# Kernel tuning notes

Measured on AMD Instinct MI355X. Metric: run time of the kernel, lower is better.

Reference implementation:

```python
import jax, jax.numpy as jnp
import numpy as np

B, T, C, H = 2, 2048, 1024, 16
HD = C // H          # head_dim = 64
HALF = HD // 2       # rope half dim = 32
ROPE_BASE = 10000.0


def _build_sin_cos(seq_len, half_dim, base=ROPE_BASE):
    # mirrors build_sin_cos: angles[t, i] = t * base^(-2i / (2*half_dim))
    pos = jnp.arange(seq_len, dtype=jnp.float32)[:, None]                     # [T,1]
    inv_freq = 1.0 / (base ** (jnp.arange(0, half_dim * 2, 2, dtype=jnp.float32) / (half_dim * 2)))
    angles = pos * inv_freq                                                   # [T, half]
    return jnp.sin(angles), jnp.cos(angles)


def setup_inputs() -> dict:
    key = jax.random.key(0)
    k1, k2, k3 = jax.random.split(key, 3)
    x = jax.random.normal(k1, (B, T, C), dtype=jnp.float32)
    # nn.Linear weights (stored as [out,in] in torch; we keep [in,out] for x @ W)
    Wqkv = jax.random.normal(k2, (C, 3 * C), dtype=jnp.float32) * (C ** -0.5)
    Wproj = jax.random.normal(k3, (C, C), dtype=jnp.float32) * (C ** -0.5)
    rope_sin, rope_cos = _build_sin_cos(T, HALF)
    return {"x": x, "Wqkv": Wqkv, "Wproj": Wproj, "rope_sin": rope_sin, "rope_cos": rope_cos}


def reference(x, Wqkv, Wproj, rope_sin, rope_cos):
    Bb, Tt, Cc = x.shape
    Hh = H
    hd = Cc // Hh
    # fused QKV projection, then per-head split (matches view(B,T,H,3*hd).split)
    qkv = (x @ Wqkv).reshape(Bb, Tt, Hh, 3 * hd)
    q, k, v = jnp.split(qkv, 3, axis=-1)                                      # each [B,T,H,hd]
    # RoPE (single device path: local slice == full range)
    s = rope_sin[:Tt][None, :, None, :].astype(x.dtype)                       # [1,T,1,half]
    c = rope_cos[:Tt][None, :, None, :].astype(x.dtype)

    def rot(t):
        t1, t2 = jnp.split(t, 2, axis=-1)
        return jnp.concatenate([t1 * c - t2 * s, t1 * s + t2 * c], axis=-1)

    q = rot(q)
    k = rot(k)
    # causal scaled dot-product attention (flash_attn default scale = hd^-0.5)
    scale = jnp.asarray(hd, x.dtype) ** -0.5
    scores = jnp.einsum('bqhd,bkhd->bhqk', q, k) * scale                      # [B,H,T,T]
    causal = jnp.tril(jnp.ones((Tt, Tt), dtype=bool))
    scores = jnp.where(causal, scores, jnp.finfo(x.dtype).min)
    probs = jax.nn.softmax(scores, axis=-1)
    attn = jnp.einsum('bhqk,bkhd->bqhd', probs, v).reshape(Bb, Tt, Cc)
    return attn @ Wproj
```

## Files before the change

### kernel.cpp

```cpp
#include <hip/hip_runtime.h>

#define Bb 2
#define Tt 2048
#define Cc_ 1024
#define Hh 16
#define HDd 64

typedef __attribute__((ext_vector_type(8))) short bf16x8;
typedef __attribute__((ext_vector_type(4))) float f32x4;
typedef __attribute__((ext_vector_type(4))) unsigned short u16x4;
typedef __attribute__((ext_vector_type(2))) unsigned int u32x2;

__device__ __forceinline__ unsigned short f2bf(float f) {
  union { float f; unsigned int u; } v; v.f = f;
  unsigned int r = v.u + 0x7FFFu + ((v.u >> 16) & 1u);
  return (unsigned short)(r >> 16);
}
__device__ __forceinline__ float bf2f(unsigned short u) {
  union { unsigned int u; float f; } v; v.u = ((unsigned int)u) << 16;
  return v.f;
}
__device__ __forceinline__ unsigned int cvtpk(float lo, float hi) {
  unsigned int r;
  asm("v_cvt_pk_bf16_f32 %0, %1, %2" : "=v"(r) : "v"(lo), "v"(hi));
  return r;
}
__device__ __forceinline__ f32x4 mfma16(bf16x8 a, bf16x8 b, f32x4 c) {
  return __builtin_amdgcn_mfma_f32_16x16x32_bf16(a, b, c, 0, 0, 0);
}
__device__ __forceinline__ void gl_lds16(const void* g, void* l) {
  auto* gp = reinterpret_cast<const __attribute__((address_space(1))) unsigned int*>(
      reinterpret_cast<unsigned long long>(g));
  auto* lp = reinterpret_cast<__attribute__((address_space(3))) unsigned int*>(
      reinterpret_cast<unsigned long long>(l));
  __builtin_amdgcn_global_load_lds(gp, lp, 16, 0, 0);
}

__global__ __launch_bounds__(256) void k_prep(const float* __restrict__ x,
                                              const float* __restrict__ Wqkv,
                                              const float* __restrict__ Wproj,
                                              unsigned short* __restrict__ xb,
                                              unsigned short* __restrict__ wqkvt,
                                              unsigned short* __restrict__ wprot) {
  const int bid = blockIdx.x;
  const int tid = threadIdx.x;
  if (bid < 4096) {
    const int i = bid * 256 + tid;
    f32x4 v = ((const f32x4*)x)[i];
    u16x4 o;
    o[0] = f2bf(v[0]); o[1] = f2bf(v[1]); o[2] = f2bf(v[2]); o[3] = f2bf(v[3]);
    ((u16x4*)xb)[i] = o;
    return;
  }
  __shared__ float tile[32][33];
  const int tx = tid & 31, ty = tid >> 5;
  if (bid < 4096 + 3072) {
    const int tt = bid - 4096;
    const int n0 = (tt % 96) * 32, k0 = (tt / 96) * 32;
    const int region = n0 >> 10, nl = n0 & 1023;
    const int ob = (nl >> 6) * 192 + region * 64 + (nl & 63);
#pragma unroll
    for (int i = 0; i < 4; ++i)
      tile[ty + i * 8][tx] = Wqkv[(size_t)(k0 + ty + i * 8) * 3072 + ob + tx];
    __syncthreads();
#pragma unroll
    for (int i = 0; i < 4; ++i)
      wqkvt[(size_t)(n0 + ty + i * 8) * 1024 + k0 + tx] = f2bf(tile[tx][ty + i * 8]);
    return;
  }
  const int tt = bid - 7168;
  const int c0 = (tt & 31) * 32, r0 = (tt >> 5) * 32;
#pragma unroll
  for (int i = 0; i < 4; ++i)
    tile[ty + i * 8][tx] = Wproj[(size_t)(r0 + ty + i * 8) * 1024 + c0 + tx];
  __syncthreads();
#pragma unroll
  for (int i = 0; i < 4; ++i)
    wprot[(size_t)(c0 + ty + i * 8) * 1024 + r0 + tx] = f2bf(tile[tx][ty + i * 8]);
}

__global__ __launch_bounds__(256) void k_gemm_qkv(const unsigned short* __restrict__ A,
                                                  const unsigned short* __restrict__ Bt,
                                                  const float* __restrict__ rsin,
                                                  const float* __restrict__ rcos,
                                                  unsigned short* __restrict__ Qo,
                                                  unsigned short* __restrict__ Ko,
                                                  unsigned short* __restrict__ Vt) {
  __shared__ unsigned short lA[2][128 * 64];
  __shared__ unsigned short lB[2][128 * 64];
  const int K = 1024;
  const int tid = threadIdx.x;
  const int lane = tid & 63, wid = tid >> 6;
  const int wr = wid >> 1, wc = wid & 1;
  const int bm = blockIdx.y * 128, bn = blockIdx.x * 128;
  const int l15 = lane & 15, l4 = lane >> 4;
  f32x4 acc[4][4];
#pragma unroll
  for (int i = 0; i < 4; ++i)
#pragma unroll
    for (int j = 0; j < 4; ++j) acc[i][j] = f32x4{0.f, 0.f, 0.f, 0.f};

#define STG(BUF, TT)                                                        \
  {                                                                         \
    const int k0 = (TT) << 6;                                               \
    _Pragma("unroll") for (int i = 0; i < 4; ++i) {                         \
      const int slot = i * 256 + tid;                                       \
      const int row = slot >> 3, g = slot & 7;                              \
      const int gs = (g ^ (row & 7)) * 8;                                   \
      gl_lds16(A + (size_t)(bm + row) * K + k0 + gs, &lA[BUF][slot * 8]);   \
      gl_lds16(Bt + (size_t)(bn + row) * K + k0 + gs, &lB[BUF][slot * 8]);  \
    }                                                                       \
  }

  STG(0, 0);
  asm volatile("s_waitcnt vmcnt(0)" ::: "memory");
  __builtin_amdgcn_s_barrier();
  for (int t = 0; t < 16; ++t) {
    const int cur = t & 1;
    if (t + 1 < 16) STG(cur ^ 1, t + 1);
    __builtin_amdgcn_s_setprio(1);
#pragma unroll
    for (int ks = 0; ks < 2; ++ks) {
      bf16x8 af[4], bfr[4];
#pragma unroll
      for (int mf = 0; mf < 4; ++mf) {
        const int row = wr * 64 + mf * 16 + l15;
        const int g = ks * 4 + l4;
        af[mf] = *(const bf16x8*)&lA[cur][row * 64 + ((g ^ (row & 7)) * 8)];
      }
#pragma unroll
      for (int nf = 0; nf < 4; ++nf) {
        const int row = wc * 64 + nf * 16 + l15;
        const int g = ks * 4 + l4;
        bfr[nf] = *(const bf16x8*)&lB[cur][row * 64 + ((g ^ (row & 7)) * 8)];
      }
#pragma unroll
      for (int mf = 0; mf < 4; ++mf)
#pragma unroll
        for (int nf = 0; nf < 4; ++nf)
          acc[mf][nf] = mfma16(af[mf], bfr[nf], acc[mf][nf]);
    }
    __builtin_amdgcn_s_setprio(0);
    if (t + 1 < 16) asm volatile("s_waitcnt vmcnt(0)" ::: "memory");
    __builtin_amdgcn_s_barrier();
  }
#undef STG

  const int rb = bm + wr * 64 + l4 * 4;
  const int region = blockIdx.x >> 3;
  if (region < 2) {
    const int h = (blockIdx.x & 7) * 2 + wc;
    unsigned short* dst = (region == 0) ? Qo : Ko;
    const float qs = (region == 0) ? (0.125f * 1.44269504088896f) : 1.0f;
#pragma unroll
    for (int mf = 0; mf < 4; ++mf)
#pragma unroll
      for (int j = 0; j < 4; ++j) {
        const int trow = rb + mf * 16 + j;
        const int bi = trow >> 11, t = trow & 2047;
        const size_t rowb = ((size_t)(bi * Hh + h) * Tt + t) * 64;
#pragma unroll
        for (int nf = 0; nf < 2; ++nf) {
          const int d = nf * 16 + l15;
          const float sn = rsin[t * 32 + d], cs = rcos[t * 32 + d];
          const float a1 = acc[mf][nf][j], a2 = acc[mf][nf + 2][j];
          dst[rowb + d] = f2bf((a1 * cs - a2 * sn) * qs);
          dst[rowb + d + 32] = f2bf((a1 * sn + a2 * cs) * qs);
        }
      }
  } else {
    unsigned short* tp = &lA[0][0];
    const int h0 = (blockIdx.x & 7) * 2;
    const int bi = bm >> 11, tbase = bm & 2047;
    const int dd = tid >> 2, t0c = (tid & 3) * 32;
#pragma unroll
    for (int ph = 0; ph < 2; ++ph) {
      if (wc == ph) {
#pragma unroll
        for (int mf = 0; mf < 4; ++mf)
#pragma unroll
          for (int nf = 0; nf < 4; ++nf)
#pragma unroll
            for (int j = 0; j < 4; ++j) {
              const int tl = wr * 64 + mf * 16 + l4 * 4 + j;
              const int dl = nf * 16 + l15;
              tp[tl * 65 + dl] = f2bf(acc[mf][nf][j]);
            }
      }
      __syncthreads();
      const size_t ob = ((size_t)(bi * Hh + h0 + ph) * 64 + dd) * (size_t)Tt + tbase + t0c;
#pragma unroll
      for (int c = 0; c < 8; ++c) {
        u16x4 v4;
#pragma unroll
        for (int e = 0; e < 4; ++e) v4[e] = tp[(t0c + c * 4 + e) * 65 + dd];
        *(u16x4*)&Vt[ob + c * 4] = v4;
      }
      __syncthreads();
    }
  }
}

__global__ __launch_bounds__(256, 4) void k_attn(const unsigned short* __restrict__ Q,
                                                 const unsigned short* __restrict__ Kt,
                                                 const unsigned short* __restrict__ Vt,
                                                 unsigned short* __restrict__ Aout) {
  __shared__ unsigned short lK[2 * 64 * 64];
  __shared__ unsigned short lV[2 * 64 * 64];
  __shared__ unsigned short lP[4 * 16 * 64];
  const int bid = blockIdx.x;
  const int xcd = bid & 7, ss = bid >> 3;
  const int cc = ss & 31, kk = ss >> 5;
  const int bh = xcd * 4 + kk;
  const int c2 = (cc + ((kk & 2) ? 16 : 0)) & 31;
  const int qt = (kk & 1) ? (31 - c2) : c2;
  const int b = bh >> 4, h = bh & 15;
  const int tid = threadIdx.x, lane = tid & 63, w = tid >> 6;
  const int l15 = lane & 15, l4 = lane >> 4;
  const int qb = qt * 64;
  const unsigned short* Kbh = Kt + (size_t)bh * Tt * 64;
  const unsigned short* Vbh = Vt + (size_t)bh * 64 * Tt;

  int fo[4][2];
#pragma unroll
  for (int a = 0; a < 4; ++a)
#pragma unroll
    for (int bb = 0; bb < 2; ++bb)
      fo[a][bb] = ((a * 16 + l15) * 64 + (((bb * 4 + l4) ^ (l15 & 7)) * 8)) * 2;
  int pwo[4];
#pragma unroll
  for (int nf = 0; nf < 4; ++nf)
    pwo[nf] = (l15 * 64 + (((nf * 2 + (l4 >> 1)) ^ (l15 & 7)) * 8) + (l4 & 1) * 4) * 2;
  char* const pB = (char*)lP + w * 2048;
  char* const kB0 = (char*)lK;
  char* const vB0 = (char*)lV;
  const int rA = tid >> 3;
  const int gsA = ((tid & 7) ^ (rA & 7)) * 8;
  const int kgA = rA * 64 + gsA;
  const int vgA = rA * 2048 + gsA;
  char* const ldKA = (char*)lK + tid * 16;
  char* const ldVA = (char*)lV + tid * 16;

#define STAGE(BUF, TT)                                                   \
  {                                                                      \
    const int kv_ = (TT) * 64;                                           \
    gl_lds16(Kbh + kv_ * 64 + kgA, ldKA + (BUF) * 8192);                 \
    gl_lds16(Kbh + kv_ * 64 + kgA + 32 * 64, ldKA + (BUF) * 8192 + 4096);\
    gl_lds16(Vbh + kv_ + vgA, ldVA + (BUF) * 8192);                      \
    gl_lds16(Vbh + kv_ + vgA + 32 * 2048, ldVA + (BUF) * 8192 + 4096);   \
  }

  const size_t qoff = ((size_t)bh * Tt + qb + w * 16 + l15) * 64 + l4 * 8;
  const bf16x8 qf0 = *(const bf16x8*)&Q[qoff];
  const bf16x8 qf1 = *(const bf16x8*)&Q[qoff + 32];
  f32x4 o[4];
#pragma unroll
  for (int i = 0; i < 4; ++i) o[i] = f32x4{0.f, 0.f, 0.f, 0.f};
  float mrun = -1e30f, lrun = 0.f;
  const int nt = qt + 1;

#define BODY(CUR, T, LASTT)                                                       \
  {                                                                               \
    if ((T) + 1 < nt) STAGE(CUR ^ 1, (T) + 1);                                    \
    f32x4 sv[4];                                                                  \
    _Pragma("unroll") for (int i = 0; i < 4; ++i) sv[i] = f32x4{0.f, 0.f, 0.f, 0.f}; \
    __builtin_amdgcn_s_setprio(1);                                                \
    _Pragma("unroll") for (int ks = 0; ks < 2; ++ks) {                            \
      const bf16x8 qa = ks ? qf1 : qf0;                                           \
      _Pragma("unroll") for (int nf = 0; nf < 4; ++nf) {                          \
        const bf16x8 kf = *(const bf16x8*)(kB0 + (CUR) * 8192 + fo[nf][ks]);      \
        sv[nf] = mfma16(kf, qa, sv[nf]);                                          \
      }                                                                           \
    }                                                                             \
    __builtin_amdgcn_s_setprio(0);                                                \
    if (LASTT) {                                                                  \
      _Pragma("unroll") for (int nf = 0; nf < 4; ++nf)                            \
        _Pragma("unroll") for (int j = 0; j < 4; ++j)                             \
          if (nf * 16 + l4 * 4 + j > w * 16 + l15) sv[nf][j] = -3e38f;            \
    }                                                                             \
    float mx = fmaxf(fmaxf(fmaxf(sv[0][0], sv[0][1]), fmaxf(sv[0][2], sv[0][3])), \
                     fmaxf(fmaxf(sv[1][0], sv[1][1]), fmaxf(sv[1][2], sv[1][3])));\
    mx = fmaxf(mx, fmaxf(fmaxf(fmaxf(sv[2][0], sv[2][1]), fmaxf(sv[2][2], sv[2][3])), \
                         fmaxf(fmaxf(sv[3][0], sv[3][1]), fmaxf(sv[3][2], sv[3][3])))); \
    if (!__all(mx - mrun <= 8.0f)) {                                              \
      mx = fmaxf(mx, __shfl_xor(mx, 16, 64));                                     \
      mx = fmaxf(mx, __shfl_xor(mx, 32, 64));                                     \
      const float mnew = fmaxf(mrun, mx);                                         \
      const float alpha = exp2f(mrun - mnew);                                     \
      lrun *= alpha;                                                              \
      float aj[4];                                                                \
      _Pragma("unroll") for (int j = 0; j < 4; ++j) aj[j] = __shfl(alpha, l4 * 4 + j, 64); \
      _Pragma("unroll") for (int df = 0; df < 4; ++df)                            \
        _Pragma("unroll") for (int j = 0; j < 4; ++j) o[df][j] *= aj[j];          \
      mrun = mnew;                                                                \
    }                                                                             \
    _Pragma("unroll") for (int nf = 0; nf < 4; ++nf) {                            \
      const float p0 = exp2f(sv[nf][0] - mrun), p1 = exp2f(sv[nf][1] - mrun);     \
      const float p2 = exp2f(sv[nf][2] - mrun), p3 = exp2f(sv[nf][3] - mrun);     \
      lrun += (p0 + p1) + (p2 + p3);                                              \
      u32x2 pk; pk[0] = cvtpk(p0, p1); pk[1] = cvtpk(p2, p3);                     \
      *(u32x2*)(pB + pwo[nf]) = pk;                                               \
    }                                                                             \
    __builtin_amdgcn_s_setprio(1);                                                \
    _Pragma("unroll") for (int kb = 0; kb < 2; ++kb) {                            \
      const bf16x8 pa = *(const bf16x8*)(pB + fo[0][kb]);                         \
      _Pragma("unroll") for (int df = 0; df < 4; ++df) {                          \
        const bf16x8 vb = *(const bf16x8*)(vB0 + (CUR) * 8192 + fo[df][kb]);      \
        o[df] = mfma16(pa, vb, o[df]);                                            \
      }                                                                           \
    }                                                                             \
    __builtin_amdgcn_s_setprio(0);                                                \
    if ((T) + 1 < nt) asm volatile("s_waitcnt vmcnt(0)" ::: "memory");            \
    __builtin_amdgcn_s_barrier();                                                 \
  }

  STAGE(0, 0);
  asm volatile("s_waitcnt vmcnt(0)" ::: "memory");
  __builtin_amdgcn_s_barrier();
  int t = 0;
  for (; t + 2 < nt; t += 2) {
    BODY(0, t, false);
    BODY(1, t + 1, false);
  }
  if (nt - t == 2) {
    BODY(0, t, false);
    BODY(1, t + 1, true);
  } else {
    BODY(0, t, true);
  }
#undef BODY
#undef STAGE

  lrun += __shfl_xor(lrun, 16, 64);
  lrun += __shfl_xor(lrun, 32, 64);
  const float rinv = 1.f / lrun;
  float lj[4];
#pragma unroll
  for (int j = 0; j < 4; ++j) lj[j] = __shfl(rinv, l4 * 4 + j, 64);
#pragma unroll
  for (int j = 0; j < 4; ++j) {
    const size_t rr = (size_t)(b * Tt + qb + w * 16 + l4 * 4 + j) * 1024 + h * 64 + l15;
#pragma unroll
    for (int df = 0; df < 4; ++df) Aout[rr + df * 16] = f2bf(o[df][j] * lj[j]);
  }
}

__global__ __launch_bounds__(256) void k_gemm2(const unsigned short* __restrict__ A,
                                               const unsigned short* __restrict__ Bt,
                                               float* __restrict__ Cout) {
  __shared__ unsigned short lA[2][128 * 64];
  __shared__ unsigned short lB[2][64 * 64];
  const int K = 1024, N = 1024;
  const int tid = threadIdx.x;
  const int lane = tid & 63, w = tid >> 6;
  const int bm = blockIdx.y * 128, bn = blockIdx.x * 64;
  const int l15 = lane & 15, l4 = lane >> 4;
  f32x4 acc[2][4];
#pragma unroll
  for (int i = 0; i < 2; ++i)
#pragma unroll
    for (int j = 0; j < 4; ++j) acc[i][j] = f32x4{0.f, 0.f, 0.f, 0.f};

#define STG(BUF, TT)                                                        \
  {                                                                         \
    const int k0 = (TT) << 6;                                               \
    _Pragma("unroll") for (int i = 0; i < 4; ++i) {                         \
      const int slot = i * 256 + tid;                                       \
      const int row = slot >> 3, g = slot & 7;                              \
      const int gs = (g ^ (row & 7)) * 8;                                   \
      gl_lds16(A + (size_t)(bm + row) * K + k0 + gs, &lA[BUF][slot * 8]);   \
    }                                                                       \
    _Pragma("unroll") for (int i = 0; i < 2; ++i) {                         \
      const int slot = i * 256 + tid;                                       \
      const int row = slot >> 3, g = slot & 7;                              \
      const int gs = (g ^ (row & 7)) * 8;                                   \
      gl_lds16(Bt + (size_t)(bn + row) * K + k0 + gs, &lB[BUF][slot * 8]);  \
    }                                                                       \
  }

  STG(0, 0);
  asm volatile("s_waitcnt vmcnt(0)" ::: "memory");
  __builtin_amdgcn_s_barrier();
  for (int t = 0; t < 16; ++t) {
    const int cur = t & 1;
    if (t + 1 < 16) STG(cur ^ 1, t + 1);
    __builtin_amdgcn_s_setprio(1);
#pragma unroll
    for (int ks = 0; ks < 2; ++ks) {
      bf16x8 af[2], bfr[4];
#pragma unroll
      for (int mf = 0; mf < 2; ++mf) {
        const int row = w * 32 + mf * 16 + l15;
        const int g = ks * 4 + l4;
        af[mf] = *(const bf16x8*)&lA[cur][row * 64 + ((g ^ (row & 7)) * 8)];
      }
#pragma unroll
      for (int nf = 0; nf < 4; ++nf) {
        const int row = nf * 16 + l15;
        const int g = ks * 4 + l4;
        bfr[nf] = *(const bf16x8*)&lB[cur][row * 64 + ((g ^ (row & 7)) * 8)];
      }
#pragma unroll
      for (int mf = 0; mf < 2; ++mf)
#pragma unroll
        for (int nf = 0; nf < 4; ++nf)
          acc[mf][nf] = mfma16(af[mf], bfr[nf], acc[mf][nf]);
    }
    __builtin_amdgcn_s_setprio(0);
    if (t + 1 < 16) asm volatile("s_waitcnt vmcnt(0)" ::: "memory");
    __builtin_amdgcn_s_barrier();
  }
#undef STG
  const int rb = bm + w * 32 + l4 * 4;
  const int cb = bn + l15;
#pragma unroll
  for (int mf = 0; mf < 2; ++mf)
#pragma unroll
    for (int nf = 0; nf < 4; ++nf)
#pragma unroll
      for (int j = 0; j < 4; ++j)
        Cout[(size_t)(rb + mf * 16 + j) * N + cb + nf * 16] = acc[mf][nf][j];
}

extern "C" void kernel_launch(void* const* d_in, const int* in_sizes, int n_in,
                              void* d_out, int out_size, void* d_ws, size_t ws_size,
                              hipStream_t stream) {
  const float* x = (const float*)d_in[0];
  const float* Wqkv = (const float*)d_in[1];
  const float* Wproj = (const float*)d_in[2];
  const float* rsin = (const float*)d_in[3];
  const float* rcos = (const float*)d_in[4];
  float* out = (float*)d_out;
  char* ws = (char*)d_ws;
  unsigned short* xb = (unsigned short*)(ws);
  unsigned short* wqkvt = (unsigned short*)(ws + (size_t)(8 << 20));
  unsigned short* wprot = (unsigned short*)(ws + (size_t)(14 << 20));
  unsigned short* Q = (unsigned short*)(ws + (size_t)(40 << 20));
  unsigned short* K = (unsigned short*)(ws + (size_t)(48 << 20));
  unsigned short* Vt = (unsigned short*)(ws + (size_t)(56 << 20));
  unsigned short* attn = (unsigned short*)(ws + (size_t)(64 << 20));

  k_prep<<<8192, 256, 0, stream>>>(x, Wqkv, Wproj, xb, wqkvt, wprot);
  k_gemm_qkv<<<dim3(24, 32), 256, 0, stream>>>(xb, wqkvt, rsin, rcos, Q, K, Vt);
  k_attn<<<1024, 256, 0, stream>>>(Q, K, Vt, attn);
  k_gemm2<<<dim3(16, 32), 256, 0, stream>>>(attn, wprot, out);
}
```

Measured before the change: 176.2 us.

## Rewrite attention kernel with 32x32 MFMA, two waves, register P exchange

Switches the attention kernel from 16x16x32 to 32x32x16 bf16 MFMA tiles, with each of two waves owning 32 query rows instead of four waves with 16 rows each. The P matrix is no longer staged through LDS; the probabilities are packed to bf16 and swapped between half-waves with a cross-lane shuffle to form the A operand for the PV product. Row statistics are broadcast through a small LDS array. The aim is to cut LDS traffic and raise MFMA efficiency. The cost is fewer waves per block, higher register pressure from the 16-wide accumulators, and less latency hiding.

Measured after the change: 192.7 us. 1.09x slower.

```diff
diff --git a/kernel.cpp b/kernel.cpp
--- a/kernel.cpp
+++ b/kernel.cpp
@@ -8,6 +8,7 @@
 
 typedef __attribute__((ext_vector_type(8))) short bf16x8;
 typedef __attribute__((ext_vector_type(4))) float f32x4;
+typedef __attribute__((ext_vector_type(16))) float f32x16;
 typedef __attribute__((ext_vector_type(4))) unsigned short u16x4;
 typedef __attribute__((ext_vector_type(2))) unsigned int u32x2;
 
@@ -27,6 +28,9 @@
 }
 __device__ __forceinline__ f32x4 mfma16(bf16x8 a, bf16x8 b, f32x4 c) {
   return __builtin_amdgcn_mfma_f32_16x16x32_bf16(a, b, c, 0, 0, 0);
+}
+__device__ __forceinline__ f32x16 mfma32(bf16x8 a, bf16x8 b, f32x16 c) {
+  return __builtin_amdgcn_mfma_f32_32x32x16_bf16(a, b, c, 0, 0, 0);
 }
 __device__ __forceinline__ void gl_lds16(const void* g, void* l) {
   auto* gp = reinterpret_cast<const __attribute__((address_space(1))) unsigned int*>(
@@ -201,13 +205,13 @@
   }
 }
 
-__global__ __launch_bounds__(256, 4) void k_attn(const unsigned short* __restrict__ Q,
+__global__ __launch_bounds__(128, 2) void k_attn(const unsigned short* __restrict__ Q,
                                                  const unsigned short* __restrict__ Kt,
                                                  const unsigned short* __restrict__ Vt,
                                                  unsigned short* __restrict__ Aout) {
   __shared__ unsigned short lK[2 * 64 * 64];
   __shared__ unsigned short lV[2 * 64 * 64];
-  __shared__ unsigned short lP[4 * 16 * 64];
+  __shared__ float sred[2][32];
   const int bid = blockIdx.x;
   const int xcd = bid & 7, ss = bid >> 3;
   const int cc = ss & 31, kk = ss >> 5;
@@ -216,102 +220,116 @@
   const int qt = (kk & 1) ? (31 - c2) : c2;
   const int b = bh >> 4, h = bh & 15;
   const int tid = threadIdx.x, lane = tid & 63, w = tid >> 6;
-  const int l15 = lane & 15, l4 = lane >> 4;
+  const int l31 = lane & 31, ht = lane >> 5, l7 = lane & 7;
   const int qb = qt * 64;
   const unsigned short* Kbh = Kt + (size_t)bh * Tt * 64;
   const unsigned short* Vbh = Vt + (size_t)bh * 64 * Tt;
 
-  int fo[4][2];
-#pragma unroll
-  for (int a = 0; a < 4; ++a)
-#pragma unroll
-    for (int bb = 0; bb < 2; ++bb)
-      fo[a][bb] = ((a * 16 + l15) * 64 + (((bb * 4 + l4) ^ (l15 & 7)) * 8)) * 2;
-  int pwo[4];
-#pragma unroll
-  for (int nf = 0; nf < 4; ++nf)
-    pwo[nf] = (l15 * 64 + (((nf * 2 + (l4 >> 1)) ^ (l15 & 7)) * 8) + (l4 & 1) * 4) * 2;
-  char* const pB = (char*)lP + w * 2048;
-  char* const kB0 = (char*)lK;
-  char* const vB0 = (char*)lV;
-  const int rA = tid >> 3;
-  const int gsA = ((tid & 7) ^ (rA & 7)) * 8;
-  const int kgA = rA * 64 + gsA;
-  const int vgA = rA * 2048 + gsA;
-  char* const ldKA = (char*)lK + tid * 16;
-  char* const ldVA = (char*)lV + tid * 16;
-
-#define STAGE(BUF, TT)                                                   \
-  {                                                                      \
-    const int kv_ = (TT) * 64;                                           \
-    gl_lds16(Kbh + kv_ * 64 + kgA, ldKA + (BUF) * 8192);                 \
-    gl_lds16(Kbh + kv_ * 64 + kgA + 32 * 64, ldKA + (BUF) * 8192 + 4096);\
-    gl_lds16(Vbh + kv_ + vgA, ldVA + (BUF) * 8192);                      \
-    gl_lds16(Vbh + kv_ + vgA + 32 * 2048, ldVA + (BUF) * 8192 + 4096);   \
-  }
-
-  const size_t qoff = ((size_t)bh * Tt + qb + w * 16 + l15) * 64 + l4 * 8;
-  const bf16x8 qf0 = *(const bf16x8*)&Q[qoff];
-  const bf16x8 qf1 = *(const bf16x8*)&Q[qoff + 32];
-  f32x4 o[4];
-#pragma unroll
-  for (int i = 0; i < 4; ++i) o[i] = f32x4{0.f, 0.f, 0.f, 0.f};
+  int off[2][4];
+#pragma unroll
+  for (int c = 0; c < 2; ++c)
+#pragma unroll
+    for (int g4 = 0; g4 < 4; ++g4)
+      off[c][g4] = (c * 32 + l31) * 64 + (((ht + g4 * 2) ^ l7) * 8);
+  const int rA = tid >> 3, gA = tid & 7;
+  const int sws = (gA ^ (rA & 7)) * 8;
+
+#define STAGE(BUF, TT)                                                              \
+  {                                                                                 \
+    const int kv_ = (TT) * 64;                                                      \
+    _Pragma("unroll") for (int i = 0; i < 4; ++i) {                                 \
+      const int row = rA + i * 16;                                                  \
+      gl_lds16(Kbh + (size_t)(kv_ + row) * 64 + sws, &lK[(BUF)*4096 + row * 64 + gA * 8]); \
+      gl_lds16(Vbh + (size_t)row * 2048 + kv_ + sws, &lV[(BUF)*4096 + row * 64 + gA * 8]); \
+    }                                                                               \
+  }
+
+  const size_t qrow_off = ((size_t)bh * Tt + qb + w * 32 + l31) * 64;
+  bf16x8 qf[4];
+#pragma unroll
+  for (int kd = 0; kd < 4; ++kd) qf[kd] = *(const bf16x8*)&Q[qrow_off + kd * 16 + ht * 8];
+
+  f32x16 o0, o1;
+#pragma unroll
+  for (int r = 0; r < 16; ++r) { o0[r] = 0.f; o1[r] = 0.f; }
   float mrun = -1e30f, lrun = 0.f;
   const int nt = qt + 1;
 
-#define BODY(CUR, T, LASTT)                                                       \
-  {                                                                               \
-    if ((T) + 1 < nt) STAGE(CUR ^ 1, (T) + 1);                                    \
-    f32x4 sv[4];                                                                  \
-    _Pragma("unroll") for (int i = 0; i < 4; ++i) sv[i] = f32x4{0.f, 0.f, 0.f, 0.f}; \
-    __builtin_amdgcn_s_setprio(1);                                                \
-    _Pragma("unroll") for (int ks = 0; ks < 2; ++ks) {                            \
-      const bf16x8 qa = ks ? qf1 : qf0;                                           \
-      _Pragma("unroll") for (int nf = 0; nf < 4; ++nf) {                          \
-        const bf16x8 kf = *(const bf16x8*)(kB0 + (CUR) * 8192 + fo[nf][ks]);      \
-        sv[nf] = mfma16(kf, qa, sv[nf]);                                          \
-      }                                                                           \
-    }                                                                             \
-    __builtin_amdgcn_s_setprio(0);                                                \
-    if (LASTT) {                                                                  \
-      _Pragma("unroll") for (int nf = 0; nf < 4; ++nf)                            \
-        _Pragma("unroll") for (int j = 0; j < 4; ++j)                             \
-          if (nf * 16 + l4 * 4 + j > w * 16 + l15) sv[nf][j] = -3e38f;            \
-    }                                                                             \
-    float mx = fmaxf(fmaxf(fmaxf(sv[0][0], sv[0][1]), fmaxf(sv[0][2], sv[0][3])), \
-                     fmaxf(fmaxf(sv[1][0], sv[1][1]), fmaxf(sv[1][2], sv[1][3])));\
-    mx = fmaxf(mx, fmaxf(fmaxf(fmaxf(sv[2][0], sv[2][1]), fmaxf(sv[2][2], sv[2][3])), \
-                         fmaxf(fmaxf(sv[3][0], sv[3][1]), fmaxf(sv[3][2], sv[3][3])))); \
-    if (!__all(mx - mrun <= 8.0f)) {                                              \
-      mx = fmaxf(mx, __shfl_xor(mx, 16, 64));                                     \
-      mx = fmaxf(mx, __shfl_xor(mx, 32, 64));                                     \
-      const float mnew = fmaxf(mrun, mx);                                         \
-      const float alpha = exp2f(mrun - mnew);                                     \
-      lrun *= alpha;                                                              \
-      float aj[4];                                                                \
-      _Pragma("unroll") for (int j = 0; j < 4; ++j) aj[j] = __shfl(alpha, l4 * 4 + j, 64); \
-      _Pragma("unroll") for (int df = 0; df < 4; ++df)                            \
-        _Pragma("unroll") for (int j = 0; j < 4; ++j) o[df][j] *= aj[j];          \
-      mrun = mnew;                                                                \
-    }                                                                             \
-    _Pragma("unroll") for (int nf = 0; nf < 4; ++nf) {                            \
-      const float p0 = exp2f(sv[nf][0] - mrun), p1 = exp2f(sv[nf][1] - mrun);     \
-      const float p2 = exp2f(sv[nf][2] - mrun), p3 = exp2f(sv[nf][3] - mrun);     \
-      lrun += (p0 + p1) + (p2 + p3);                                              \
-      u32x2 pk; pk[0] = cvtpk(p0, p1); pk[1] = cvtpk(p2, p3);                     \
-      *(u32x2*)(pB + pwo[nf]) = pk;                                               \
-    }                                                                             \
-    __builtin_amdgcn_s_setprio(1);                                                \
-    _Pragma("unroll") for (int kb = 0; kb < 2; ++kb) {                            \
-      const bf16x8 pa = *(const bf16x8*)(pB + fo[0][kb]);                         \
-      _Pragma("unroll") for (int df = 0; df < 4; ++df) {                          \
-        const bf16x8 vb = *(const bf16x8*)(vB0 + (CUR) * 8192 + fo[df][kb]);      \
-        o[df] = mfma16(pa, vb, o[df]);                                            \
-      }                                                                           \
-    }                                                                             \
-    __builtin_amdgcn_s_setprio(0);                                                \
-    if ((T) + 1 < nt) asm volatile("s_waitcnt vmcnt(0)" ::: "memory");            \
-    __builtin_amdgcn_s_barrier();                                                 \
+#define BODY(CUR, T, LASTT)                                                             \
+  {                                                                                     \
+    if ((T) + 1 < nt) STAGE(CUR ^ 1, (T) + 1);                                          \
+    f32x16 s0, s1;                                                                      \
+    _Pragma("unroll") for (int r = 0; r < 16; ++r) { s0[r] = 0.f; s1[r] = 0.f; }        \
+    __builtin_amdgcn_s_setprio(1);                                                      \
+    _Pragma("unroll") for (int kd = 0; kd < 4; ++kd) {                                  \
+      const bf16x8 k0 = *(const bf16x8*)&lK[(CUR)*4096 + off[0][kd]];                   \
+      const bf16x8 k1 = *(const bf16x8*)&lK[(CUR)*4096 + off[1][kd]];                   \
+      s0 = mfma32(k0, qf[kd], s0);                                                      \
+      s1 = mfma32(k1, qf[kd], s1);                                                      \
+    }                                                                                   \
+    __builtin_amdgcn_s_setprio(0);                                                      \
+    if (LASTT) {                                                                        \
+      const int qr = w * 32 + l31;                                                      \
+      _Pragma("unroll") for (int r = 0; r < 16; ++r) {                                  \
+        const int key0 = (r & 3) + 8 * (r >> 2) + 4 * ht;                               \
+        if (key0 > qr) s0[r] = -3e38f;                                                  \
+        if (32 + key0 > qr) s1[r] = -3e38f;                                             \
+      }                                                                                 \
+    }                                                                                   \
+    float mx = fmaxf(s0[0], s1[0]);                                                     \
+    _Pragma("unroll") for (int r = 1; r < 16; ++r) mx = fmaxf(mx, fmaxf(s0[r], s1[r])); \
+    mx = fmaxf(mx, __shfl_xor(mx, 32, 64));                                             \
+    if (!__all(mx - mrun <= 8.0f)) {                                                    \
+      const float mnew = fmaxf(mrun, mx);                                               \
+      const float alpha = exp2f(mrun - mnew);                                           \
+      lrun *= alpha;                                                                    \
+      if (lane < 32) sred[w][l31] = alpha;                                              \
+      _Pragma("unroll") for (int r = 0; r < 16; ++r) {                                  \
+        const float av = sred[w][(r & 3) + 8 * (r >> 2) + 4 * ht];                      \
+        o0[r] *= av; o1[r] *= av;                                                       \
+      }                                                                                 \
+      mrun = mnew;                                                                      \
+    }                                                                                   \
+    float ssum = 0.f;                                                                   \
+    _Pragma("unroll") for (int r = 0; r < 16; ++r) {                                    \
+      const float p0 = exp2f(s0[r] - mrun), p1 = exp2f(s1[r] - mrun);                   \
+      ssum += p0 + p1; s0[r] = p0; s1[r] = p1;                                          \
+    }                                                                                   \
+    lrun += ssum;                                                                       \
+    unsigned int u0[8], u1[8];                                                          \
+    _Pragma("unroll") for (int rr = 0; rr < 8; ++rr) {                                  \
+      u0[rr] = cvtpk(s0[2 * rr], s0[2 * rr + 1]);                                       \
+      u1[rr] = cvtpk(s1[2 * rr], s1[2 * rr + 1]);                                       \
+    }                                                                                   \
+    unsigned int rc0[4], rc1[4];                                                        \
+    _Pragma("unroll") for (int jj = 0; jj < 4; ++jj) {                                  \
+      const int a = (jj >> 1) * 4 + (jj & 1);                                           \
+      rc0[jj] = __shfl_xor((int)(ht ? u0[a] : u0[a + 2]), 32, 64);                      \
+      rc1[jj] = __shfl_xor((int)(ht ? u1[a] : u1[a + 2]), 32, 64);                      \
+    }                                                                                   \
+    __builtin_amdgcn_s_setprio(1);                                                      \
+    _Pragma("unroll") for (int ks = 0; ks < 4; ++ks) {                                  \
+      const int b4 = (ks & 1) * 4, b2 = (ks & 1) * 2;                                   \
+      union { unsigned int u[4]; bf16x8 v; } pa;                                        \
+      if (ks < 2) {                                                                     \
+        pa.u[0] = ht ? rc0[b2] : u0[b4];                                                \
+        pa.u[1] = ht ? rc0[b2 + 1] : u0[b4 + 1];                                        \
+        pa.u[2] = ht ? u0[b4 + 2] : rc0[b2];                                            \
+        pa.u[3] = ht ? u0[b4 + 3] : rc0[b2 + 1];                                        \
+      } else {                                                                          \
+        pa.u[0] = ht ? rc1[b2] : u1[b4];                                                \
+        pa.u[1] = ht ? rc1[b2 + 1] : u1[b4 + 1];                                        \
+        pa.u[2] = ht ? u1[b4 + 2] : rc1[b2];                                            \
+        pa.u[3] = ht ? u1[b4 + 3] : rc1[b2 + 1];                                        \
+      }                                                                                 \
+      const bf16x8 vb0 = *(const bf16x8*)&lV[(CUR)*4096 + off[0][ks]];                  \
+      const bf16x8 vb1 = *(const bf16x8*)&lV[(CUR)*4096 + off[1][ks]];                  \
+      o0 = mfma32(pa.v, vb0, o0);                                                       \
+      o1 = mfma32(pa.v, vb1, o1);                                                       \
+    }                                                                                   \
+    __builtin_amdgcn_s_setprio(0);                                                      \
+    if ((T) + 1 < nt) asm volatile("s_waitcnt vmcnt(0)" ::: "memory");                  \
+    __builtin_amdgcn_s_barrier();                                                       \
   }
 
   STAGE(0, 0);
@@ -331,17 +349,15 @@
 #undef BODY
 #undef STAGE
 
-  lrun += __shfl_xor(lrun, 16, 64);
   lrun += __shfl_xor(lrun, 32, 64);
-  const float rinv = 1.f / lrun;
-  float lj[4];
-#pragma unroll
-  for (int j = 0; j < 4; ++j) lj[j] = __shfl(rinv, l4 * 4 + j, 64);
-#pragma unroll
-  for (int j = 0; j < 4; ++j) {
-    const size_t rr = (size_t)(b * Tt + qb + w * 16 + l4 * 4 + j) * 1024 + h * 64 + l15;
-#pragma unroll
-    for (int df = 0; df < 4; ++df) Aout[rr + df * 16] = f2bf(o[df][j] * lj[j]);
+  if (lane < 32) sred[w][l31] = 1.f / lrun;
+  const size_t outb = (size_t)(b * Tt + qb + w * 32) * 1024 + h * 64;
+#pragma unroll
+  for (int r = 0; r < 16; ++r) {
+    const int q = (r & 3) + 8 * (r >> 2) + 4 * ht;
+    const float li = sred[w][q];
+    Aout[outb + (size_t)q * 1024 + l31] = f2bf(o0[r] * li);
+    Aout[outb + (size_t)q * 1024 + 32 + l31] = f2bf(o1[r] * li);
   }
 }
 
@@ -442,6 +458,6 @@
 
   k_prep<<<8192, 256, 0, stream>>>(x, Wqkv, Wproj, xb, wqkvt, wprot);
   k_gemm_qkv<<<dim3(24, 32), 256, 0, stream>>>(xb, wqkvt, rsin, rcos, Q, K, Vt);
-  k_attn<<<1024, 256, 0, stream>>>(Q, K, Vt, attn);
+  k_attn<<<1024, 128, 0, stream>>>(Q, K, Vt, attn);
   k_gemm2<<<dim3(16, 32), 256, 0, stream>>>(attn, wprot, out);
 }
```
